# Kernel optimization log

Measured on AMD Instinct MI355X. Metric: run time of the kernel, lower is better.

## Reference

```python
import jax, jax.numpy as jnp
import numpy as np

NUM_NODES = 1024
INPUT_DIM = 64
HID_DIM = 64
MAX_DIFFUSION_STEP = 2
NUM_SUPPORTS = 2
OUT_DIM = 128
INPUT_SIZE = INPUT_DIM + HID_DIM          # F = 128
NUM_MATRICES = NUM_SUPPORTS * MAX_DIFFUSION_STEP + 1  # M = 5
BATCH = 64


def setup_inputs() -> dict:
    key = jax.random.key(0)
    k1, k2, k3, k4 = jax.random.split(key, 4)
    # scale supports like a normalized random-walk matrix so diffusion stays bounded
    supports = jax.random.normal(k1, (NUM_SUPPORTS, NUM_NODES, NUM_NODES), jnp.float32) / np.float32(np.sqrt(NUM_NODES))
    inputs = jax.random.normal(k2, (BATCH, NUM_NODES * INPUT_DIM), jnp.float32)
    state = jax.random.normal(k3, (BATCH, NUM_NODES * HID_DIM), jnp.float32)
    weight = jax.random.normal(k4, (INPUT_SIZE * NUM_MATRICES, OUT_DIM), jnp.float32) * 0.05
    biases = jnp.zeros((OUT_DIM,), jnp.float32)
    return {"supports": supports, "inputs": inputs, "state": state,
            "weight": weight, "biases": biases, "output_size": OUT_DIM}


def reference(supports, inputs, state, weight, biases, output_size):
    B = inputs.shape[0]
    x_in = inputs.reshape(B, NUM_NODES, -1)   # [B, N, input_dim]
    st = state.reshape(B, NUM_NODES, -1)      # [B, N, hid_dim]
    x0 = jnp.concatenate([x_in, st], axis=2)  # [B, N, F]

    xs = [x0]
    # Chebyshev-style diffusion: x_k = 2*A@x_{k-1} - x_{k-2}, per support
    for s in range(NUM_SUPPORTS):
        A = supports[s]
        x1 = jnp.einsum('nm,bmf->bnf', A, x0)
        xs.append(x1)
        xp2, xp1 = x0, x1
        for _ in range(2, MAX_DIFFUSION_STEP + 1):
            x2 = 2.0 * jnp.einsum('nm,bmf->bnf', A, xp1) - xp2
            xs.append(x2)
            xp2, xp1 = xp1, x2

    # torch does stack on dim1 -> [B,M,N,F], transpose to [B,N,F,M], reshape to F*M.
    # stacking on the last axis gives [B,N,F,M] directly (same memory order f*M+m).
    x = jnp.stack(xs, axis=3)                               # [B, N, F, M]
    x = x.reshape(B * NUM_NODES, INPUT_SIZE * NUM_MATRICES)  # [B*N, F*M]
    out = x @ weight + biases                                # [B*N, output_size]
    return out.reshape(B, NUM_NODES * output_size)
```

## Files before the change

kernel.cpp:

```cpp
#include <hip/hip_runtime.h>
#include <hip/hip_bf16.h>


typedef short bf16x8  __attribute__((ext_vector_type(8)));
typedef short short4v __attribute__((ext_vector_type(4)));
typedef float f32x4   __attribute__((ext_vector_type(4)));

constexpr size_t MB1    = 1024ull * 1024ull;
constexpr size_t SZ_MAT = 8192ull * 1024ull;
constexpr size_t OFF_PSTK = 0;
constexpr size_t OFF_SUPT = 4 * MB1;
constexpr size_t OFF_X0T  = 6 * MB1;
constexpr size_t OFF_X0NF = OFF_X0T  + SZ_MAT;
constexpr size_t OFF_XNF  = OFF_X0NF + SZ_MAT;
constexpr size_t OFF_W2T  = OFF_XNF  + 4 * SZ_MAT;

__device__ __forceinline__ unsigned short f2bf(float x) {
  union { float f; unsigned int u; } v; v.f = x;
  unsigned int r = v.u + 0x7fffu + ((v.u >> 16) & 1u);
  return (unsigned short)(r >> 16);
}

#define GLD16(gp, lp)                                                         \
  __builtin_amdgcn_global_load_lds(                                           \
      (const __attribute__((address_space(1))) unsigned int*)(gp),            \
      (__attribute__((address_space(3))) unsigned int*)(lp), 16, 0, 0)


__global__ __launch_bounds__(256)
void prep_kernel(const float* __restrict__ sup,
                 const float* __restrict__ weight,
                 const float* __restrict__ inputs,
                 const float* __restrict__ state,
                 unsigned short* __restrict__ ws) {
  __shared__ unsigned short tile[64][65];
  int bid = blockIdx.x;
  int tl  = threadIdx.x;

  if (bid < 2048) {
    size_t t = (size_t)bid * 256 + tl;
    const float4* src = (const float4*)sup;
    float4 v = src[t];
    size_t e = t * 4;
    size_t s = e >> 20;
    size_t r = e & (MB1 - 1);
    short4v o; o[0] = (short)f2bf(v.x); o[1] = (short)f2bf(v.y);
    o[2] = (short)f2bf(v.z); o[3] = (short)f2bf(v.w);
    *(short4v*)&ws[OFF_PSTK + 2 * s * MB1 + r] = o;
  } else if (bid < 2560) {
    int i = bid - 2048;
    int nt = i & 15, mt = (i >> 4) & 15, s = i >> 8;
    const float* A = sup + (size_t)s * MB1;
    unsigned short* AT = ws + OFF_SUPT + (size_t)s * MB1;
    int cl = tl & 63, rg = tl >> 6;
#pragma unroll 4
    for (int rr = 0; rr < 16; ++rr) {
      int rl = rr * 4 + rg;
      tile[rl][cl] = f2bf(A[(size_t)(nt * 64 + rl) * 1024 + mt * 64 + cl]);
    }
    __syncthreads();
#pragma unroll 4
    for (int rr = 0; rr < 16; ++rr) {
      int ml = rr * 4 + rg;
      AT[(size_t)(mt * 64 + ml) * 1024 + nt * 64 + cl] = tile[cl][ml];
    }
  } else if (bid < 2880) {
    int t = (bid - 2560) * 256 + tl;
    int o = t / 640, k = t % 640;
    int m = k >> 7, f = k & 127;
    ws[OFF_W2T + t] = f2bf(weight[(f * 5 + m) * 128 + o]);
  } else {
    int i = bid - 2880;
    int b = i & 63, nt = (i >> 6) & 15, ft = i >> 10;
    const float* src = ft ? state : inputs;
    unsigned short* x0t  = ws + OFF_X0T;
    unsigned short* x0nf = ws + OFF_X0NF;
    int fl = tl & 63, nr = tl >> 6;
#pragma unroll 4
    for (int rr = 0; rr < 16; ++rr) {
      int n_loc = rr * 4 + nr;
      float v = src[(size_t)b * 65536 + (size_t)(nt * 64 + n_loc) * 64 + fl];
      unsigned short bv = f2bf(v);
      tile[n_loc][fl] = bv;
      x0nf[(size_t)(nt * 64 + n_loc) * 8192 + b * 128 + ft * 64 + fl] = bv;
    }
    __syncthreads();
#pragma unroll 4
    for (int rr = 0; rr < 16; ++rr) {
      int f_loc = rr * 4 + nr;
      x0t[(size_t)(b * 128 + ft * 64 + f_loc) * 1024 + nt * 64 + fl] =
          tile[fl][f_loc];
    }
  }
}


template <int MODE, int NJ>
__global__ __launch_bounds__(256)
void gemm_kernel(unsigned short* __restrict__ ws,
                 const float* __restrict__ bias,
                 float* __restrict__ dout) {
  __shared__ short At[128 * 64];
  __shared__ short Bt[32 * NJ * 64];

  const int tid = threadIdx.x;
  const int l   = tid & 63;
  const int w   = tid >> 6;
  const int wr  = w >> 1, wc = w & 1;

  int bm, bn, s = 0;
  const unsigned short* A = nullptr;
  const unsigned short* B;
  int KT;
  if constexpr (MODE == 0) {
    bm = blockIdx.x; bn = blockIdx.y; s = blockIdx.z;
    A = ws + OFF_PSTK + (size_t)(2 * s) * MB1;
    B = ws + OFF_SUPT + (size_t)s * MB1;
    KT = 16;
  } else if constexpr (MODE == 1) {
    int bid = blockIdx.x;
    int xcd = bid & 7, idx = bid >> 3;
    bm = ((xcd & 1) << 4) | (idx & 15);
    bn = ((xcd >> 1) << 4) | (idx >> 4);
    A = ws + OFF_PSTK;
    B = ws + OFF_X0T;
    KT = 16;
  } else {
    bm = blockIdx.x; bn = 0;
    B = ws + OFF_W2T;
    KT = 10;
  }

  const int subrow = l >> 3;
  const int koff   = (((l & 7) << 3) ^ (subrow << 3));

  f32x4 acc[4][NJ] = {};

  for (int kt = 0; kt < KT; ++kt) {
#pragma unroll
    for (int c = 0; c < 4; ++c) {
      int chunk = w * 4 + c;
      int rowl  = chunk * 8 + subrow;
      const unsigned short* gp;
      if constexpr (MODE == 2) {
        int rg = bm * 128 + rowl;
        const unsigned short* base =
            (kt < 2) ? (ws + OFF_X0NF)
                     : (ws + OFF_XNF + (size_t)((kt >> 1) - 1) * SZ_MAT);
        gp = base + (size_t)(rg >> 6) * 8192 + (size_t)(rg & 63) * 128 +
             (kt & 1) * 64 + koff;
      } else {
        gp = A + (size_t)(bm * 128 + rowl) * 1024 + kt * 64 + koff;
      }
      GLD16(gp, &At[chunk * 512]);
    }
#pragma unroll
    for (int c = 0; c < NJ; ++c) {
      int chunk = w * NJ + c;
      int rowl  = chunk * 8 + subrow;
      const unsigned short* gp;
      if constexpr (MODE == 2) {
        gp = B + (size_t)rowl * 640 + kt * 64 + koff;
      } else {
        gp = B + (size_t)(bn * (32 * NJ) + rowl) * 1024 + kt * 64 + koff;
      }
      GLD16(gp, &Bt[chunk * 512]);
    }
    __syncthreads();

#pragma unroll
    for (int kk = 0; kk < 2; ++kk) {
      bf16x8 af[4], bfv[NJ];
#pragma unroll
      for (int i = 0; i < 4; ++i) {
        int row = wr * 64 + i * 16 + (l & 15);
        int off = row * 64 + ((kk * 32 + ((l >> 4) << 3)) ^ ((row & 7) << 3));
        af[i] = *(const bf16x8*)&At[off];
      }
#pragma unroll
      for (int j = 0; j < NJ; ++j) {
        int row = wc * (16 * NJ) + j * 16 + (l & 15);
        int off = row * 64 + ((kk * 32 + ((l >> 4) << 3)) ^ ((row & 7) << 3));
        bfv[j] = *(const bf16x8*)&Bt[off];
      }
#pragma unroll
      for (int i = 0; i < 4; ++i)
#pragma unroll
        for (int j = 0; j < NJ; ++j)
          acc[i][j] = __builtin_amdgcn_mfma_f32_16x16x32_bf16(af[i], bfv[j],
                                                              acc[i][j], 0, 0, 0);
    }
    __syncthreads();
  }

  if constexpr (MODE == 0) {
    unsigned short* P = ws + OFF_PSTK + (size_t)(2 * s + 1) * MB1;
#pragma unroll
    for (int i = 0; i < 4; ++i) {
      int rg0 = bm * 128 + wr * 64 + i * 16 + ((l >> 4) << 2);
#pragma unroll
      for (int j = 0; j < NJ; ++j) {
        int cg = bn * (32 * NJ) + wc * (16 * NJ) + j * 16 + (l & 15);
#pragma unroll
        for (int r = 0; r < 4; ++r) {
          int rg = rg0 + r;
          float v = 2.0f * acc[i][j][r] - (rg == cg ? 1.0f : 0.0f);
          P[(size_t)rg * 1024 + cg] = f2bf(v);
        }
      }
    }
  } else if constexpr (MODE == 1) {
    unsigned short* Y = ws + OFF_XNF;
#pragma unroll
    for (int i = 0; i < 4; ++i) {
      int rg0 = bm * 128 + wr * 64 + i * 16 + ((l >> 4) << 2);
#pragma unroll
      for (int j = 0; j < NJ; ++j) {
        int cg = bn * 128 + wc * 64 + j * 16 + (l & 15);
#pragma unroll
        for (int r = 0; r < 4; ++r)
          Y[(size_t)(rg0 + r) * 8192 + cg] = f2bf(acc[i][j][r]);
      }
    }
  } else {
#pragma unroll
    for (int i = 0; i < 4; ++i) {
      int rg0 = bm * 128 + wr * 64 + i * 16 + ((l >> 4) << 2);
#pragma unroll
      for (int j = 0; j < NJ; ++j) {
        int cg = wc * 64 + j * 16 + (l & 15);
        float bv = bias[cg];
#pragma unroll
        for (int r = 0; r < 4; ++r) {
          int rg = rg0 + r;
          int drow = ((rg & 63) << 10) | (rg >> 6);
          dout[(size_t)drow * 128 + cg] = acc[i][j][r] + bv;
        }
      }
    }
  }
}


extern "C" void kernel_launch(void* const* d_in, const int* in_sizes, int n_in,
                              void* d_out, int out_size, void* d_ws, size_t ws_size,
                              hipStream_t stream) {
  (void)in_sizes; (void)n_in; (void)out_size; (void)ws_size;
  const float* supports = (const float*)d_in[0];
  const float* inputs   = (const float*)d_in[1];
  const float* state    = (const float*)d_in[2];
  const float* weight   = (const float*)d_in[3];
  const float* bias     = (const float*)d_in[4];
  float* out = (float*)d_out;
  unsigned short* ws = (unsigned short*)d_ws;

  prep_kernel<<<4928, 256, 0, stream>>>(supports, weight, inputs, state, ws);
  gemm_kernel<0, 1><<<dim3(8, 32, 2), 256, 0, stream>>>(ws, bias, out);
  gemm_kernel<1, 4><<<2048, 256, 0, stream>>>(ws, bias, out);
  gemm_kernel<2, 4><<<512, 256, 0, stream>>>(ws, bias, out);
}
```

Before: 127.9 us.

## Fuse diffusion GEMM and output projection into one kernel keeping intermediates in LDS

Replaces the separate diffusion GEMM (which wrote four 16MB bf16 intermediate tensors to global memory) and the final projection GEMM with a single kernel. Each block computes a 128x128 tile of each diffusion band and stages it in LDS as bf16. It then immediately multiplies that tile by the matching weight slice, accumulating the output in registers. This removes the global round trip of the intermediates and one kernel launch. In exchange each block now runs a long serial band loop with 64KB dynamic LDS, which may limit occupancy, and the x0 tile is reloaded once per band.

After: 113.7 us. 1.12x faster.

```diff
diff --git a/kernel.cpp b/kernel.cpp
--- a/kernel.cpp
+++ b/kernel.cpp
@@ -95,148 +95,258 @@
 }
 
 
-template <int MODE, int NJ>
-__global__ __launch_bounds__(256)
-void gemm_kernel(unsigned short* __restrict__ ws,
+__global__ __launch_bounds__(256, 2)
+void mega_kernel(unsigned short* __restrict__ ws,
                  const float* __restrict__ bias,
                  float* __restrict__ dout) {
-  __shared__ short At[128 * 64];
-  __shared__ short Bt[32 * NJ * 64];
+  extern __shared__ unsigned short lds[];
+
+  const unsigned short* X0T = ws + OFF_X0T;
+  const unsigned short* X0N = ws + OFF_X0NF;
+  const unsigned short* W2  = ws + OFF_W2T;
 
   const int tid = threadIdx.x;
   const int l   = tid & 63;
   const int w   = tid >> 6;
   const int wr  = w >> 1, wc = w & 1;
-
-  int bm, bn, s = 0;
-  const unsigned short* A = nullptr;
-  const unsigned short* B;
-  int KT;
-  if constexpr (MODE == 0) {
-    bm = blockIdx.x; bn = blockIdx.y; s = blockIdx.z;
-    A = ws + OFF_PSTK + (size_t)(2 * s) * MB1;
-    B = ws + OFF_SUPT + (size_t)s * MB1;
-    KT = 16;
-  } else if constexpr (MODE == 1) {
-    int bid = blockIdx.x;
-    int xcd = bid & 7, idx = bid >> 3;
-    bm = ((xcd & 1) << 4) | (idx & 15);
-    bn = ((xcd >> 1) << 4) | (idx >> 4);
-    A = ws + OFF_PSTK;
-    B = ws + OFF_X0T;
-    KT = 16;
-  } else {
-    bm = blockIdx.x; bn = 0;
-    B = ws + OFF_W2T;
-    KT = 10;
-  }
+  const int lm  = l & 15, q = l >> 4;
+
+  int bid = blockIdx.x;
+  int xcd = bid & 7, idx = bid >> 3;
+  const int bm = xcd * 8 + (idx & 7);
+  const int bn = idx >> 3;
 
   const int subrow = l >> 3;
   const int koff   = (((l & 7) << 3) ^ (subrow << 3));
 
-  f32x4 acc[4][NJ] = {};
-
-  for (int kt = 0; kt < KT; ++kt) {
-#pragma unroll
-    for (int c = 0; c < 4; ++c) {
-      int chunk = w * 4 + c;
-      int rowl  = chunk * 8 + subrow;
-      const unsigned short* gp;
-      if constexpr (MODE == 2) {
-        int rg = bm * 128 + rowl;
-        const unsigned short* base =
-            (kt < 2) ? (ws + OFF_X0NF)
-                     : (ws + OFF_XNF + (size_t)((kt >> 1) - 1) * SZ_MAT);
-        gp = base + (size_t)(rg >> 6) * 8192 + (size_t)(rg & 63) * 128 +
-             (kt & 1) * 64 + koff;
-      } else {
-        gp = A + (size_t)(bm * 128 + rowl) * 1024 + kt * 64 + koff;
-      }
-      GLD16(gp, &At[chunk * 512]);
-    }
-#pragma unroll
-    for (int c = 0; c < NJ; ++c) {
-      int chunk = w * NJ + c;
-      int rowl  = chunk * 8 + subrow;
-      const unsigned short* gp;
-      if constexpr (MODE == 2) {
-        gp = B + (size_t)rowl * 640 + kt * 64 + koff;
-      } else {
-        gp = B + (size_t)(bn * (32 * NJ) + rowl) * 1024 + kt * 64 + koff;
-      }
-      GLD16(gp, &Bt[chunk * 512]);
-    }
-    __syncthreads();
-
+  auto stage_x0t = [&](int kt) {
+#pragma unroll
+    for (int c = 0; c < 4; ++c) {
+      int chunk = w * 4 + c, rowl = chunk * 8 + subrow;
+      const unsigned short* gp =
+          X0T + (size_t)(bm * 128 + rowl) * 1024 + kt * 64 + koff;
+      GLD16(gp, &lds[chunk * 512]);
+    }
+  };
+  auto stage_P = [&](int band, int kt) {
+#pragma unroll
+    for (int c = 0; c < 4; ++c) {
+      int chunk = w * 4 + c, rowl = chunk * 8 + subrow;
+      const unsigned short* gp = ws + OFF_PSTK + (size_t)band * MB1 +
+                                 (size_t)(bn * 128 + rowl) * 1024 + kt * 64 + koff;
+      GLD16(gp, &lds[8192 + chunk * 512]);
+    }
+  };
+  auto stage_w2 = [&](int m, int kt2) {
+#pragma unroll
+    for (int c = 0; c < 4; ++c) {
+      int chunk = w * 4 + c, rowl = chunk * 8 + subrow;
+      const unsigned short* gp =
+          W2 + (size_t)rowl * 640 + m * 128 + kt2 * 64 + koff;
+      GLD16(gp, &lds[chunk * 512]);
+    }
+  };
+  auto stage_x0n = [&](int kt2) {
+#pragma unroll
+    for (int c = 0; c < 4; ++c) {
+      int chunk = w * 4 + c, rowl = chunk * 8 + subrow;
+      const unsigned short* gp =
+          X0N + (size_t)(bn * 128 + rowl) * 8192 + bm * 128 + kt2 * 64 + koff;
+      GLD16(gp, &lds[8192 + chunk * 512]);
+    }
+  };
+
+  f32x4 oacc[4][4] = {};
+
+  for (int band = 0; band < 4; ++band) {
+    f32x4 yacc[4][4] = {};
+    for (int kt = 0; kt < 16; ++kt) {
+      stage_x0t(kt);
+      stage_P(band, kt);
+      __syncthreads();
+#pragma unroll
+      for (int kk = 0; kk < 2; ++kk) {
+        bf16x8 af[4], bfv[4];
+#pragma unroll
+        for (int i = 0; i < 4; ++i) {
+          int row = wr * 64 + i * 16 + lm;
+          int off = row * 64 + ((kk * 32 + (q << 3)) ^ ((row & 7) << 3));
+          af[i] = *(const bf16x8*)&lds[off];
+        }
+#pragma unroll
+        for (int j = 0; j < 4; ++j) {
+          int row = wc * 64 + j * 16 + lm;
+          int off = 8192 + row * 64 + ((kk * 32 + (q << 3)) ^ ((row & 7) << 3));
+          bfv[j] = *(const bf16x8*)&lds[off];
+        }
+#pragma unroll
+        for (int i = 0; i < 4; ++i)
+#pragma unroll
+          for (int j = 0; j < 4; ++j)
+            yacc[i][j] = __builtin_amdgcn_mfma_f32_16x16x32_bf16(
+                af[i], bfv[j], yacc[i][j], 0, 0, 0);
+      }
+      __syncthreads();
+    }
+
+#pragma unroll
+    for (int i = 0; i < 4; ++i) {
+      int f0 = wr * 64 + i * 16 + q * 4;
+#pragma unroll
+      for (int j = 0; j < 4; ++j) {
+        int n = wc * 64 + j * 16 + lm;
+        short4v pk;
+#pragma unroll
+        for (int r = 0; r < 4; ++r) pk[r] = (short)f2bf(yacc[i][j][r]);
+        *(short4v*)&lds[16384 + n * 128 + (((f0 >> 3) ^ (n & 7)) << 3) +
+                        (f0 & 7)] = pk;
+      }
+    }
+    __syncthreads();
+
+#pragma unroll
+    for (int kt2 = 0; kt2 < 2; ++kt2) {
+      stage_w2(band + 1, kt2);
+      __syncthreads();
+#pragma unroll
+      for (int kk = 0; kk < 2; ++kk) {
+        bf16x8 af[4], bfv[4];
+#pragma unroll
+        for (int i = 0; i < 4; ++i) {
+          int row = wr * 64 + i * 16 + lm;
+          int off = row * 64 + ((kk * 32 + (q << 3)) ^ ((row & 7) << 3));
+          af[i] = *(const bf16x8*)&lds[off];
+        }
+#pragma unroll
+        for (int j = 0; j < 4; ++j) {
+          int n = wc * 64 + j * 16 + lm;
+          int g = kt2 * 8 + kk * 4 + q;
+          bfv[j] = *(const bf16x8*)&lds[16384 + n * 128 + ((g ^ (n & 7)) << 3)];
+        }
+#pragma unroll
+        for (int i = 0; i < 4; ++i)
+#pragma unroll
+          for (int j = 0; j < 4; ++j)
+            oacc[i][j] = __builtin_amdgcn_mfma_f32_16x16x32_bf16(
+                af[i], bfv[j], oacc[i][j], 0, 0, 0);
+      }
+      __syncthreads();
+    }
+  }
+
+#pragma unroll
+  for (int kt2 = 0; kt2 < 2; ++kt2) {
+    stage_w2(0, kt2);
+    stage_x0n(kt2);
+    __syncthreads();
 #pragma unroll
     for (int kk = 0; kk < 2; ++kk) {
-      bf16x8 af[4], bfv[NJ];
+      bf16x8 af[4], bfv[4];
+#pragma unroll
+      for (int i = 0; i < 4; ++i) {
+        int row = wr * 64 + i * 16 + lm;
+        int off = row * 64 + ((kk * 32 + (q << 3)) ^ ((row & 7) << 3));
+        af[i] = *(const bf16x8*)&lds[off];
+      }
+#pragma unroll
+      for (int j = 0; j < 4; ++j) {
+        int row = wc * 64 + j * 16 + lm;
+        int off = 8192 + row * 64 + ((kk * 32 + (q << 3)) ^ ((row & 7) << 3));
+        bfv[j] = *(const bf16x8*)&lds[off];
+      }
+#pragma unroll
+      for (int i = 0; i < 4; ++i)
+#pragma unroll
+        for (int j = 0; j < 4; ++j)
+          oacc[i][j] = __builtin_amdgcn_mfma_f32_16x16x32_bf16(
+              af[i], bfv[j], oacc[i][j], 0, 0, 0);
+    }
+    __syncthreads();
+  }
+
+#pragma unroll
+  for (int i = 0; i < 4; ++i) {
+    int o0 = wr * 64 + i * 16 + q * 4;
+    float4 bv = *(const float4*)&bias[o0];
+#pragma unroll
+    for (int j = 0; j < 4; ++j) {
+      int n = bn * 128 + wc * 64 + j * 16 + lm;
+      float4 v;
+      v.x = oacc[i][j][0] + bv.x;
+      v.y = oacc[i][j][1] + bv.y;
+      v.z = oacc[i][j][2] + bv.z;
+      v.w = oacc[i][j][3] + bv.w;
+      *(float4*)&dout[(size_t)bm * 131072 + (size_t)n * 128 + o0] = v;
+    }
+  }
+}
+
+
+__global__ __launch_bounds__(256)
+void psq_kernel(unsigned short* __restrict__ ws) {
+  __shared__ short At[128 * 64];
+  __shared__ short Bt[32 * 64];
+
+  const int tid = threadIdx.x;
+  const int l   = tid & 63;
+  const int w   = tid >> 6;
+  const int wr  = w >> 1, wc = w & 1;
+
+  const int bm = blockIdx.x, bn = blockIdx.y, s = blockIdx.z;
+  const unsigned short* A = ws + OFF_PSTK + (size_t)(2 * s) * MB1;
+  const unsigned short* B = ws + OFF_SUPT + (size_t)s * MB1;
+
+  const int subrow = l >> 3;
+  const int koff   = (((l & 7) << 3) ^ (subrow << 3));
+
+  f32x4 acc[4][1] = {};
+
+  for (int kt = 0; kt < 16; ++kt) {
+#pragma unroll
+    for (int c = 0; c < 4; ++c) {
+      int chunk = w * 4 + c, rowl = chunk * 8 + subrow;
+      GLD16(A + (size_t)(bm * 128 + rowl) * 1024 + kt * 64 + koff,
+            &At[chunk * 512]);
+    }
+    {
+      int chunk = w, rowl = chunk * 8 + subrow;
+      GLD16(B + (size_t)(bn * 32 + rowl) * 1024 + kt * 64 + koff,
+            &Bt[chunk * 512]);
+    }
+    __syncthreads();
+
+#pragma unroll
+    for (int kk = 0; kk < 2; ++kk) {
+      bf16x8 af[4], bfv;
 #pragma unroll
       for (int i = 0; i < 4; ++i) {
         int row = wr * 64 + i * 16 + (l & 15);
         int off = row * 64 + ((kk * 32 + ((l >> 4) << 3)) ^ ((row & 7) << 3));
         af[i] = *(const bf16x8*)&At[off];
       }
-#pragma unroll
-      for (int j = 0; j < NJ; ++j) {
-        int row = wc * (16 * NJ) + j * 16 + (l & 15);
+      {
+        int row = wc * 16 + (l & 15);
         int off = row * 64 + ((kk * 32 + ((l >> 4) << 3)) ^ ((row & 7) << 3));
-        bfv[j] = *(const bf16x8*)&Bt[off];
+        bfv = *(const bf16x8*)&Bt[off];
       }
 #pragma unroll
       for (int i = 0; i < 4; ++i)
-#pragma unroll
-        for (int j = 0; j < NJ; ++j)
-          acc[i][j] = __builtin_amdgcn_mfma_f32_16x16x32_bf16(af[i], bfv[j],
-                                                              acc[i][j], 0, 0, 0);
-    }
-    __syncthreads();
-  }
-
-  if constexpr (MODE == 0) {
-    unsigned short* P = ws + OFF_PSTK + (size_t)(2 * s + 1) * MB1;
-#pragma unroll
-    for (int i = 0; i < 4; ++i) {
-      int rg0 = bm * 128 + wr * 64 + i * 16 + ((l >> 4) << 2);
-#pragma unroll
-      for (int j = 0; j < NJ; ++j) {
-        int cg = bn * (32 * NJ) + wc * (16 * NJ) + j * 16 + (l & 15);
-#pragma unroll
-        for (int r = 0; r < 4; ++r) {
-          int rg = rg0 + r;
-          float v = 2.0f * acc[i][j][r] - (rg == cg ? 1.0f : 0.0f);
-          P[(size_t)rg * 1024 + cg] = f2bf(v);
-        }
-      }
-    }
-  } else if constexpr (MODE == 1) {
-    unsigned short* Y = ws + OFF_XNF;
-#pragma unroll
-    for (int i = 0; i < 4; ++i) {
-      int rg0 = bm * 128 + wr * 64 + i * 16 + ((l >> 4) << 2);
-#pragma unroll
-      for (int j = 0; j < NJ; ++j) {
-        int cg = bn * 128 + wc * 64 + j * 16 + (l & 15);
-#pragma unroll
-        for (int r = 0; r < 4; ++r)
-          Y[(size_t)(rg0 + r) * 8192 + cg] = f2bf(acc[i][j][r]);
-      }
-    }
-  } else {
-#pragma unroll
-    for (int i = 0; i < 4; ++i) {
-      int rg0 = bm * 128 + wr * 64 + i * 16 + ((l >> 4) << 2);
-#pragma unroll
-      for (int j = 0; j < NJ; ++j) {
-        int cg = wc * 64 + j * 16 + (l & 15);
-        float bv = bias[cg];
-#pragma unroll
-        for (int r = 0; r < 4; ++r) {
-          int rg = rg0 + r;
-          int drow = ((rg & 63) << 10) | (rg >> 6);
-          dout[(size_t)drow * 128 + cg] = acc[i][j][r] + bv;
-        }
-      }
+        acc[i][0] = __builtin_amdgcn_mfma_f32_16x16x32_bf16(af[i], bfv,
+                                                            acc[i][0], 0, 0, 0);
+    }
+    __syncthreads();
+  }
+
+  unsigned short* P = ws + OFF_PSTK + (size_t)(2 * s + 1) * MB1;
+#pragma unroll
+  for (int i = 0; i < 4; ++i) {
+    int rg0 = bm * 128 + wr * 64 + i * 16 + ((l >> 4) << 2);
+    int cg  = bn * 32 + wc * 16 + (l & 15);
+#pragma unroll
+    for (int r = 0; r < 4; ++r) {
+      int rg = rg0 + r;
+      float v = 2.0f * acc[i][0][r] - (rg == cg ? 1.0f : 0.0f);
+      P[(size_t)rg * 1024 + cg] = f2bf(v);
     }
   }
 }
@@ -255,7 +365,6 @@
   unsigned short* ws = (unsigned short*)d_ws;
 
   prep_kernel<<<4928, 256, 0, stream>>>(supports, weight, inputs, state, ws);
-  gemm_kernel<0, 1><<<dim3(8, 32, 2), 256, 0, stream>>>(ws, bias, out);
-  gemm_kernel<1, 4><<<2048, 256, 0, stream>>>(ws, bias, out);
-  gemm_kernel<2, 4><<<512, 256, 0, stream>>>(ws, bias, out);
-}
+  psq_kernel<<<dim3(8, 32, 2), 256, 0, stream>>>(ws);
+  mega_kernel<<<512, 256, 65536, stream>>>(ws, bias, out);
+}
```
